# Kernel optimization log

Hardware: AMD Instinct MI355X
Metric: run time of the kernel (lower is better)

The kernel has to match this reference:

```python
import jax, jax.numpy as jnp
import numpy as np

# wav2vec2 feature-extractor conv stack config: (kernel, stride) per layer, 512 channels
CONV_CFG = [(10, 5), (3, 2), (3, 2), (3, 2), (3, 2), (2, 2), (2, 2)]
C = 512
PROJ = 256
HID = 128
NCLS = 5
N_WORDS = 64
B = 8
L = 40000


def _conv1d(h, w, stride):
    # h: [B, Cin, T], w: [Cout, Cin, K]
    return jax.lax.conv_general_dilated(
        h, w, window_strides=(stride,), padding='VALID',
        dimension_numbers=('NCH', 'OIH', 'NCH'))


def setup_inputs() -> dict:
    key = jax.random.key(0)
    ks = jax.random.split(key, 16)
    x = jax.random.normal(ks[0], (B, L), dtype=jnp.float32)
    word_ids = jax.random.randint(ks[1], (B,), 0, N_WORDS)
    convs = {}
    cin = 1
    for i, (k, s) in enumerate(CONV_CFG):
        fan = cin * k
        convs[f'conv{i}'] = jax.random.normal(ks[2 + i], (C, cin, k), dtype=jnp.float32) / np.sqrt(fan)
        cin = C
    gn_scale = jnp.ones((C,), dtype=jnp.float32)
    gn_bias = jnp.zeros((C,), dtype=jnp.float32)
    proj_w = jax.random.normal(ks[9], (PROJ, C), dtype=jnp.float32) / np.sqrt(C)
    proj_b = jnp.zeros((PROJ,), dtype=jnp.float32)
    cls_w1 = jax.random.normal(ks[10], (N_WORDS, PROJ, HID), dtype=jnp.float32) / np.sqrt(PROJ)
    cls_b1 = jnp.zeros((N_WORDS, HID), dtype=jnp.float32)
    cls_w2 = jax.random.normal(ks[11], (N_WORDS, HID, NCLS), dtype=jnp.float32) / np.sqrt(HID)
    cls_b2 = jnp.zeros((N_WORDS, NCLS), dtype=jnp.float32)
    return dict(x=x, word_ids=word_ids, gn_scale=gn_scale, gn_bias=gn_bias,
                proj_w=proj_w, proj_b=proj_b, cls_w1=cls_w1, cls_b1=cls_b1,
                cls_w2=cls_w2, cls_b2=cls_b2, **convs)


def _forward(x, convs, gn_scale, gn_bias, proj_w, proj_b, cls_w1, cls_b1, cls_w2, cls_b2, word_ids):
    h = x[:, None, :]  # [B,1,L]
    for i, (k, s) in enumerate(CONV_CFG):
        h = _conv1d(h, convs[i], s)
        if i == 0:
            # wav2vec2 group-norm: groups == channels -> per-channel norm over time
            mu = jnp.mean(h, axis=-1, keepdims=True)
            var = jnp.var(h, axis=-1, keepdims=True)
            h = (h - mu) * jax.lax.rsqrt(var + 1e-5)
            h = h * gn_scale[None, :, None] + gn_bias[None, :, None]
        h = jax.nn.gelu(h)
    feat = jnp.mean(h, axis=-1)                          # [B, 512] mean-pool over time
    feat = jax.nn.relu(feat @ proj_w.T + proj_b)         # [B, 256] (dropout = identity in eval)
    w1 = cls_w1[word_ids]                                # [B, 256, 128] routed gather
    h1 = jax.nn.relu(jnp.einsum('bd,bdh->bh', feat, w1) + cls_b1[word_ids])
    out = jnp.einsum('bh,bho->bo', h1, cls_w2[word_ids]) + cls_b2[word_ids]  # [B, 5]
    return out


def reference(x, word_ids, gn_scale, gn_bias, proj_w, proj_b, cls_w1, cls_b1, cls_w2, cls_b2,
              conv0, conv1, conv2, conv3, conv4, conv5, conv6):
    convs = [conv0, conv1, conv2, conv3, conv4, conv5, conv6]
    return _forward(x, convs, gn_scale, gn_bias, proj_w, proj_b,
                    cls_w1, cls_b1, cls_w2, cls_b2, word_ids)
```

## Files before the change

kernel.cpp:

```cpp
#include <hip/hip_runtime.h>
#include <hip/hip_bf16.h>

typedef unsigned short u16;
typedef short bf16x8 __attribute__((ext_vector_type(8)));
typedef float f32x4 __attribute__((ext_vector_type(4)));

#define CC 512

__device__ __forceinline__ float gelu_tanh(float x) {
    float x3 = x * x * x;
    float z  = 0.7978845608028654f * (x + 0.044715f * x3);
    float e  = __expf(2.0f * z);
    float th = 1.0f - 2.0f / (e + 1.0f);
    return 0.5f * x * (1.0f + th);
}

__device__ __forceinline__ u16 f2bf(float f) {
    union { float f; unsigned u; } v; v.f = f;
    unsigned r = v.u + 0x7fff + ((v.u >> 16) & 1);
    return (u16)(r >> 16);
}
__device__ __forceinline__ float bf2f(u16 h) {
    union { unsigned u; float f; } v; v.u = ((unsigned)h) << 16; return v.f;
}

__global__ __launch_bounds__(256) void conv0_store(
    const float* __restrict__ x, const float* __restrict__ w0,
    u16* __restrict__ actG, float* __restrict__ part) {
    const int t0 = blockIdx.x * 64, b = blockIdx.y;
    __shared__ float xs[64 * 5 + 16];
    __shared__ float w0t[10 * 512];
    for (int i = threadIdx.x; i < 64 * 5 + 5; i += 256) {
        int gi = t0 * 5 + i;
        xs[i] = (gi < 40000) ? x[b * 40000 + gi] : 0.0f;
    }
    for (int i = threadIdx.x; i < 5120; i += 256) {
        int c = i / 10, j = i - c * 10;
        w0t[j * 512 + c] = w0[i];
    }
    __syncthreads();
    const int lane = threadIdx.x & 63, wv = threadIdx.x >> 6;
    float wr[8][10];
#pragma unroll
    for (int q = 0; q < 8; ++q)
#pragma unroll
        for (int j = 0; j < 10; ++j) wr[q][j] = w0t[j * 512 + lane + 64 * q];
    float sacc[8] = {}, qacc[8] = {};
    u16* ob = actG + ((size_t)b * 8320 + t0 + wv * 16) * 512 + lane;
#pragma unroll
    for (int u = 0; u < 16; ++u) {
        const int tt = wv * 16 + u;
        const int t  = t0 + tt;
        float xv[10];
#pragma unroll
        for (int j = 0; j < 10; ++j) xv[j] = xs[tt * 5 + j];
#pragma unroll
        for (int q = 0; q < 8; ++q) {
            float a = 0.0f;
#pragma unroll
            for (int j = 0; j < 10; ++j) a = fmaf(wr[q][j], xv[j], a);
            const u16 h = f2bf(a);
            ob[(size_t)u * 512 + 64 * q] = h;
            if (t < 7999) {
                const float ar = bf2f(h);
                sacc[q] += ar; qacc[q] += ar * ar;
            }
        }
    }
    float* pp = part + ((((size_t)blockIdx.x * 4 + wv) * 8 + b) * 512 + lane) * 2;
#pragma unroll
    for (int q = 0; q < 8; ++q) {
        pp[q * 128] = sacc[q]; pp[q * 128 + 1] = qacc[q];
    }
}

__global__ __launch_bounds__(256) void stats_finalizeAB(
    const float* __restrict__ part, const float* __restrict__ gsc,
    const float* __restrict__ gbi, float* __restrict__ Af, float* __restrict__ Bf) {
    const int row = blockIdx.x * 256 + threadIdx.x;
    float s = 0.0f, q = 0.0f;
    for (int k = 0; k < 500; ++k) {
        const float2 v = *(const float2*)(part + ((size_t)k * 4096 + row) * 2);
        s += v.x; q += v.y;
    }
    float mean = s / 7999.0f;
    float var  = fmaxf(q / 7999.0f - mean * mean, 0.0f);
    float rstd = rsqrtf(var + 1e-5f);
    const int c = row & (CC - 1);
    float A = rstd * gsc[c];
    Af[row] = A;
    Bf[row] = gbi[c] - mean * A;
}

__global__ __launch_bounds__(256) void gn_apply(
    u16* __restrict__ actG, const float* __restrict__ Af,
    const float* __restrict__ Bf) {
    const int b = blockIdx.y;
    const int idx = blockIdx.x * 256 + threadIdx.x;
    const int row = idx >> 6, c0 = (idx & 63) * 8;
    if (row >= 7999) return;
    u16* p = actG + ((size_t)b * 8320 + row) * 512 + c0;
    union { u16 s[8]; uint4 v; } in, outv;
    in.v = *(const uint4*)p;
    const float4 a0 = *(const float4*)(Af + b * 512 + c0);
    const float4 a1 = *(const float4*)(Af + b * 512 + c0 + 4);
    const float4 b0 = *(const float4*)(Bf + b * 512 + c0);
    const float4 b1 = *(const float4*)(Bf + b * 512 + c0 + 4);
    const float av[8] = {a0.x, a0.y, a0.z, a0.w, a1.x, a1.y, a1.z, a1.w};
    const float bv[8] = {b0.x, b0.y, b0.z, b0.w, b1.x, b1.y, b1.z, b1.w};
#pragma unroll
    for (int e = 0; e < 8; ++e)
        outv.s[e] = f2bf(gelu_tanh(fmaf(bf2f(in.s[e]), av[e], bv[e])));
    *(uint4*)p = outv.v;
}

template <int K, int NL>
struct WtBatch { const float* src[NL]; u16* dst[NL]; };

template <int K, int NL>
__global__ __launch_bounds__(256) void wt_transform(WtBatch<K, NL> a) {
    constexpr int WROW = 32 * K + 8;
    const int cit = blockIdx.x, cob = blockIdx.y, l = blockIdx.z;
    const float* w = a.src[l];
    u16* dst = a.dst[l] + ((size_t)(cob * 16 + cit)) * 128 * WROW;
    for (int idx = threadIdx.x; idx < 128 * WROW; idx += 256) {
        const int co = idx / WROW, e = idx - co * WROW;
        u16 hi = 0;
        if (e < 32 * K) {
            const int j = e >> 5, ci = e & 31;
            hi = f2bf(w[((size_t)(cob * 128 + co) * 512 + cit * 32 + ci) * K + j]);
        }
        dst[idx] = hi;
    }
}

template <int K, int TT>
__global__ __launch_bounds__(256, 2) void conv_mfma(
    const u16* __restrict__ act, int capIn,
    const u16* __restrict__ wt,
    u16* __restrict__ outAct, int capOut, int tbShift) {
    constexpr int WROW = 32 * K + 8;
    constexpr int XH   = TT + 8;
    constexpr int TF   = TT / 32;
    constexpr int NXCH = XH * 8;
    constexpr int NWCH = 128 * WROW / 8;
    constexpr int NKX  = (NXCH + 255) / 256;
    constexpr int NKW  = (NWCH + 255) / 256;

    __shared__ __align__(16) u16 Xs[XH * 64];
    __shared__ __align__(16) u16 Ws[128 * WROW];

    const int tid  = threadIdx.x;
    const int lane = tid & 63;
    const int wv   = tid >> 6;
    const int wco  = wv >> 1, wtt = wv & 1;
    const int l15  = lane & 15, l16 = lane >> 4;

    const int flat = blockIdx.x;
    const int xcd  = flat & 7, cob = (flat >> 3) & 3;
    const int G    = xcd + (flat >> 5) * 8;
    const int t_b  = G & ((1 << tbShift) - 1);
    const int b    = G >> tbShift;
    const int t0   = t_b * TT;
    const int x0   = t0 * 2;

    const char* abase = (const char*)(act + (size_t)b * capIn * 512);
    const u16*  wbase = wt + (size_t)cob * (16 * 128 * WROW);

    const char* xsrc[NKX]; int xdst[NKX]; bool xok[NKX];
#pragma unroll
    for (int k = 0; k < NKX; ++k) {
        const int cb = wv * 64 + k * 256;
        xok[k] = (cb < NXCH);
        const int c  = cb + lane;
        const int xh = c >> 3;
        const int li = ((c & 7) * 16) ^ ((xh & 7) << 4);
        const int xx = min(x0 + 2 * xh + (li >> 6), capIn - 1);
        xsrc[k] = abase + (size_t)xx * 1024 + (li & 63);
        xdst[k] = cb * 16;
    }
    const char* wsrc[NKW]; int wdst[NKW]; bool wok[NKW];
#pragma unroll
    for (int k = 0; k < NKW; ++k) {
        const int cb = wv * 64 + k * 256;
        wok[k] = (cb < NWCH);
        wsrc[k] = (const char*)wbase + (size_t)(cb + lane) * 16;
        wdst[k] = cb * 16;
    }

    auto stageAll = [&]() {
#pragma unroll
        for (int k = 0; k < NKX; ++k)
            if (xok[k])
                __builtin_amdgcn_global_load_lds(
                    (const __attribute__((address_space(1))) void*)xsrc[k],
                    (__attribute__((address_space(3))) void*)((char*)&Xs[0] + xdst[k]),
                    16, 0, 0);
#pragma unroll
        for (int k = 0; k < NKW; ++k)
            if (wok[k])
                __builtin_amdgcn_global_load_lds(
                    (const __attribute__((address_space(1))) void*)wsrc[k],
                    (__attribute__((address_space(3))) void*)((char*)&Ws[0] + wdst[k]),
                    16, 0, 0);
#pragma unroll
        for (int k = 0; k < NKX; ++k) xsrc[k] += 64;
#pragma unroll
        for (int k = 0; k < NKW; ++k) wsrc[k] += 128 * WROW * 2;
    };

    int xoff[K][TF];
    int woff[K][4];
#pragma unroll
    for (int j = 0; j < K; ++j) {
#pragma unroll
        for (int tf = 0; tf < TF; ++tf) {
            const int tl = wtt * (TT / 2) + tf * 16 + l15;
            const int xl = 2 * tl + j;
            const int xh = xl >> 1, p = xl & 1;
            xoff[j][tf] = xh * 128 + ((p * 64 + l16 * 16) ^ ((xh & 7) << 4));
        }
#pragma unroll
        for (int cf = 0; cf < 4; ++cf)
            woff[j][cf] = (wco * 64 + cf * 16 + l15) * WROW + j * 32 + l16 * 8;
    }

    f32x4 acc[4][TF] = {};

    stageAll();
    __syncthreads();

#pragma unroll 1
    for (int cit = 0; cit < 16; ++cit) {
        bf16x8 xr[K][TF], wr[K][4];
#pragma unroll
        for (int j = 0; j < K; ++j) {
#pragma unroll
            for (int tf = 0; tf < TF; ++tf)
                xr[j][tf] = *(const bf16x8*)((const char*)&Xs[0] + xoff[j][tf]);
#pragma unroll
            for (int cf = 0; cf < 4; ++cf)
                wr[j][cf] = *(const bf16x8*)(&Ws[0] + woff[j][cf]);
        }
        __syncthreads();
        if (cit < 15) stageAll();
#pragma unroll
        for (int j = 0; j < K; ++j)
#pragma unroll
            for (int cf = 0; cf < 4; ++cf)
#pragma unroll
                for (int tf = 0; tf < TF; ++tf)
                    acc[cf][tf] = __builtin_amdgcn_mfma_f32_16x16x32_bf16(
                        wr[j][cf], xr[j][tf], acc[cf][tf], 0, 0, 0);
        __syncthreads();
    }

    u16* ob = outAct + (size_t)b * capOut * 512;
#pragma unroll
    for (int cf = 0; cf < 4; ++cf) {
#pragma unroll
        for (int tf = 0; tf < TF; ++tf) {
            const int tG  = t0 + wtt * (TT / 2) + tf * 16 + l15;
            const int coG = cob * 128 + wco * 64 + cf * 16 + l16 * 4;
            union { u16 s[4]; uint2 v; } pk;
#pragma unroll
            for (int r = 0; r < 4; ++r)
                pk.s[r] = f2bf(gelu_tanh(acc[cf][tf][r]));
            *(uint2*)(ob + (size_t)tG * 512 + coG) = pk.v;
        }
    }
}

__global__ __launch_bounds__(512) void feat_proj_kernel(
    const u16* __restrict__ act, int cap,
    const float* __restrict__ pw, const float* __restrict__ pb,
    float* __restrict__ pfeat) {
    const int b = blockIdx.x;
    __shared__ float fs[8][512];
    __shared__ float feat[CC];
    const int c8 = (threadIdx.x & 63) * 8;
    const int tg = threadIdx.x >> 6;
    float s[8] = {};
    for (int t = tg; t < 124; t += 8) {
        union { u16 u[8]; uint4 v; } in;
        in.v = *(const uint4*)(act + ((size_t)b * cap + t) * 512 + c8);
#pragma unroll
        for (int e = 0; e < 8; ++e) s[e] += bf2f(in.u[e]);
    }
#pragma unroll
    for (int e = 0; e < 8; ++e) fs[tg][c8 + e] = s[e];
    __syncthreads();
    {
        const int c = threadIdx.x;
        if (c < 512) {
            float acc = 0.0f;
#pragma unroll
            for (int g = 0; g < 8; ++g) acc += fs[g][c];
            feat[c] = acc * (1.0f / 124.0f);
        }
    }
    __syncthreads();
    if (threadIdx.x < 256) {
        const int j = threadIdx.x;
        const float* wr = pw + (size_t)j * CC;
        float acc = pb[j];
        for (int cc = 0; cc < CC; ++cc) acc = fmaf(feat[cc], wr[cc], acc);
        pfeat[b * 256 + j] = fmaxf(acc, 0.0f);
    }
}

__global__ __launch_bounds__(128) void cls_kernel(
    const float* __restrict__ pfeat, const int* __restrict__ wid,
    const float* __restrict__ w1, const float* __restrict__ b1,
    const float* __restrict__ w2, const float* __restrict__ b2,
    float* __restrict__ out) {
    const int b = blockIdx.x;
    const int id = wid[b];
    __shared__ float pf[256], h1[128];
    for (int d = threadIdx.x; d < 256; d += 128) pf[d] = pfeat[b * 256 + d];
    __syncthreads();
    {
        const int hh = threadIdx.x;
        const float* w1p = w1 + (size_t)id * 256 * 128;
        float s = b1[id * 128 + hh];
        for (int d = 0; d < 256; ++d) s = fmaf(pf[d], w1p[d * 128 + hh], s);
        h1[hh] = fmaxf(s, 0.0f);
    }
    __syncthreads();
    if (threadIdx.x < 5) {
        const float* w2p = w2 + (size_t)id * 128 * 5;
        float s = b2[id * 5 + threadIdx.x];
        for (int hh = 0; hh < 128; ++hh) s = fmaf(h1[hh], w2p[hh * 5 + threadIdx.x], s);
        out[b * 5 + threadIdx.x] = s;
    }
}

extern "C" void kernel_launch(void* const* d_in, const int* in_sizes, int n_in,
                              void* d_out, int out_size, void* d_ws, size_t ws_size,
                              hipStream_t stream) {
    const float* x   = (const float*)d_in[0];
    const int*   wid = (const int*)d_in[1];
    const float* gsc = (const float*)d_in[2];
    const float* gbi = (const float*)d_in[3];
    const float* pw  = (const float*)d_in[4];
    const float* pb  = (const float*)d_in[5];
    const float* w1  = (const float*)d_in[6];
    const float* b1  = (const float*)d_in[7];
    const float* w2  = (const float*)d_in[8];
    const float* b2  = (const float*)d_in[9];
    const float* cw[7];
    for (int i = 0; i < 7; ++i) cw[i] = (const float*)d_in[10 + i];

    char* ws = (char*)d_ws;
    const size_t SZ_ACTG = (size_t)8 * 8320 * 512 * 2;
    const size_t SZ_P    = (size_t)8 * 4224 * 512 * 2;
    const size_t SZ_Q    = (size_t)8 * 2176 * 512 * 2;
    u16* actG = (u16*)ws;
    u16* bufP = (u16*)(ws + SZ_ACTG);
    u16* bufQ = (u16*)(ws + SZ_ACTG + SZ_P);
    size_t off = SZ_ACTG + SZ_P + SZ_Q;
    u16* wtbuf[7];
    for (int i = 1; i <= 4; ++i) { wtbuf[i] = (u16*)(ws + off); off += (size_t)4 * 16 * 128 * 104 * 2; }
    for (int i = 5; i <= 6; ++i) { wtbuf[i] = (u16*)(ws + off); off += (size_t)4 * 16 * 128 * 72 * 2; }
    off = (off + 255) & ~(size_t)255;
    float* statsPart = (float*)(ws + off); off += (size_t)500 * 8 * 512 * 2 * 4;
    float* Af        = (float*)(ws + off); off += 4096 * 4;
    float* Bf        = (float*)(ws + off); off += 4096 * 4;
    float* pfeat     = (float*)(ws + off); off += 8 * 256 * 4;

    conv0_store<<<dim3(125, 8), 256, 0, stream>>>(x, cw[0], actG, statsPart);
    stats_finalizeAB<<<dim3(16), 256, 0, stream>>>(statsPart, gsc, gbi, Af, Bf);
    gn_apply<<<dim3(2000, 8), 256, 0, stream>>>(actG, Af, Bf);

    {
        WtBatch<3, 4> a;
        for (int i = 0; i < 4; ++i) { a.src[i] = cw[1 + i]; a.dst[i] = wtbuf[1 + i]; }
        wt_transform<3, 4><<<dim3(16, 4, 4), 256, 0, stream>>>(a);
        WtBatch<2, 2> c;
        for (int i = 0; i < 2; ++i) { c.src[i] = cw[5 + i]; c.dst[i] = wtbuf[5 + i]; }
        wt_transform<2, 2><<<dim3(16, 4, 2), 256, 0, stream>>>(c);
    }

    conv_mfma<3, 128><<<dim3(32 * 32), 256, 0, stream>>>(actG, 8320, wtbuf[1], bufP, 4224, 5);
    conv_mfma<3, 128><<<dim3(16 * 32), 256, 0, stream>>>(bufP, 4224, wtbuf[2], bufQ, 2176, 4);
    conv_mfma<3,  64><<<dim3(16 * 32), 256, 0, stream>>>(bufQ, 2176, wtbuf[3], bufP, 4224, 4);
    conv_mfma<3,  64><<<dim3( 8 * 32), 256, 0, stream>>>(bufP, 4224, wtbuf[4], bufQ, 2176, 3);
    conv_mfma<2,  64><<<dim3( 4 * 32), 256, 0, stream>>>(bufQ, 2176, wtbuf[5], bufP, 4224, 2);
    conv_mfma<2,  64><<<dim3( 2 * 32), 256, 0, stream>>>(bufP, 4224, wtbuf[6], bufQ, 2176, 1);

    feat_proj_kernel<<<dim3(8), 512, 0, stream>>>(bufQ, 2176, pw, pb, pfeat);
    cls_kernel<<<dim3(8), 128, 0, stream>>>(pfeat, wid, w1, b1, w2, b2, (float*)d_out);
}
```

Measured before the change: 317.8 us.

## Double-buffer activation tiles and use fine-grained vmcnt waits in conv MFMA loop

Splits the activation LDS tile into two buffers so the next-next input-channel chunk of X is prefetched while the current chunk is consumed. Replaces the per-iteration __syncthreads with explicit lgkmcnt/vmcnt waits plus raw barriers, letting outstanding X loads stay in flight across iterations. It also repartitions the async global-to-LDS copy work evenly across waves. This doubles X LDS use, which may affect occupancy at 2 blocks per CU, and the hand-computed vmcnt immediate must match the issue order.

```diff
diff --git a/kernel.cpp b/kernel.cpp
--- a/kernel.cpp
+++ b/kernel.cpp
@@ -6,6 +6,10 @@
 typedef float f32x4 __attribute__((ext_vector_type(4)));
 
 #define CC 512
+
+constexpr int vmimm(int n) {
+    return (n & 0xF) | ((n >> 4) << 14) | (0x7 << 4) | (0xF << 8);
+}
 
 __device__ __forceinline__ float gelu_tanh(float x) {
     float x3 = x * x * x;
@@ -142,12 +146,16 @@
     constexpr int WROW = 32 * K + 8;
     constexpr int XH   = TT + 8;
     constexpr int TF   = TT / 32;
-    constexpr int NXCH = XH * 8;
-    constexpr int NWCH = 128 * WROW / 8;
-    constexpr int NKX  = (NXCH + 255) / 256;
-    constexpr int NKW  = (NWCH + 255) / 256;
-
-    __shared__ __align__(16) u16 Xs[XH * 64];
+    constexpr int TXC  = XH * 8;
+    constexpr int CPX  = TXC / 4;
+    constexpr int NIX  = (CPX + 63) / 64;
+    constexpr int XLAST = CPX - (NIX - 1) * 64;
+    constexpr int TWC  = 128 * WROW / 8;
+    constexpr int CPW  = TWC / 4;
+    constexpr int NIW  = (CPW + 63) / 64;
+    constexpr int WLAST = CPW - (NIW - 1) * 64;
+
+    __shared__ __align__(16) u16 Xs[2][XH * 64];
     __shared__ __align__(16) u16 Ws[128 * WROW];
 
     const int tid  = threadIdx.x;
@@ -167,46 +175,45 @@
     const char* abase = (const char*)(act + (size_t)b * capIn * 512);
     const u16*  wbase = wt + (size_t)cob * (16 * 128 * WROW);
 
-    const char* xsrc[NKX]; int xdst[NKX]; bool xok[NKX];
-#pragma unroll
-    for (int k = 0; k < NKX; ++k) {
-        const int cb = wv * 64 + k * 256;
-        xok[k] = (cb < NXCH);
-        const int c  = cb + lane;
+    const char* xsA[NIX]; const char* xsB[NIX]; int xdst[NIX];
+#pragma unroll
+    for (int i = 0; i < NIX; ++i) {
+        const int c  = wv * CPX + i * 64 + lane;
         const int xh = c >> 3;
         const int li = ((c & 7) * 16) ^ ((xh & 7) << 4);
         const int xx = min(x0 + 2 * xh + (li >> 6), capIn - 1);
-        xsrc[k] = abase + (size_t)xx * 1024 + (li & 63);
-        xdst[k] = cb * 16;
-    }
-    const char* wsrc[NKW]; int wdst[NKW]; bool wok[NKW];
-#pragma unroll
-    for (int k = 0; k < NKW; ++k) {
-        const int cb = wv * 64 + k * 256;
-        wok[k] = (cb < NWCH);
-        wsrc[k] = (const char*)wbase + (size_t)(cb + lane) * 16;
-        wdst[k] = cb * 16;
-    }
-
-    auto stageAll = [&]() {
-#pragma unroll
-        for (int k = 0; k < NKX; ++k)
-            if (xok[k])
+        xsA[i] = abase + (size_t)xx * 1024 + (li & 63);
+        xsB[i] = xsA[i] + 64;
+        xdst[i] = (wv * CPX + i * 64) * 16;
+    }
+    const char* wsrc[NIW]; int wdst[NIW];
+#pragma unroll
+    for (int i = 0; i < NIW; ++i) {
+        wsrc[i] = (const char*)wbase + (size_t)(wv * CPW + i * 64 + lane) * 16;
+        wdst[i] = (wv * CPW + i * 64) * 16;
+    }
+
+    auto stageX = [&](const char* (&xs)[NIX], u16* xb) {
+#pragma unroll
+        for (int i = 0; i < NIX; ++i)
+            if (i < NIX - 1 || lane < XLAST)
                 __builtin_amdgcn_global_load_lds(
-                    (const __attribute__((address_space(1))) void*)xsrc[k],
-                    (__attribute__((address_space(3))) void*)((char*)&Xs[0] + xdst[k]),
+                    (const __attribute__((address_space(1))) void*)xs[i],
+                    (__attribute__((address_space(3))) void*)((char*)xb + xdst[i]),
                     16, 0, 0);
 #pragma unroll
-        for (int k = 0; k < NKW; ++k)
-            if (wok[k])
+        for (int i = 0; i < NIX; ++i) xs[i] += 128;
+    };
+    auto stageW = [&]() {
+#pragma unroll
+        for (int i = 0; i < NIW; ++i)
+            if (i < NIW - 1 || lane < WLAST)
                 __builtin_amdgcn_global_load_lds(
-                    (const __attribute__((address_space(1))) void*)wsrc[k],
-                    (__attribute__((address_space(3))) void*)((char*)&Ws[0] + wdst[k]),
+                    (const __attribute__((address_space(1))) void*)wsrc[i],
+                    (__attribute__((address_space(3))) void*)((char*)&Ws[0] + wdst[i]),
                     16, 0, 0);
 #pragma unroll
-        for (int k = 0; k < NKX; ++k) xsrc[k] += 64;
-#pragma unroll
-        for (int k = 0; k < NKW; ++k) wsrc[k] += 128 * WROW * 2;
+        for (int i = 0; i < NIW; ++i) wsrc[i] += WROW * 256;
     };
 
     int xoff[K][TF];
@@ -222,28 +229,31 @@
         }
 #pragma unroll
         for (int cf = 0; cf < 4; ++cf)
-            woff[j][cf] = (wco * 64 + cf * 16 + l15) * WROW + j * 32 + l16 * 8;
+            woff[j][cf] = ((wco * 64 + cf * 16 + l15) * WROW + j * 32 + l16 * 8) * 2;
     }
 
     f32x4 acc[4][TF] = {};
 
-    stageAll();
-    __syncthreads();
-
-#pragma unroll 1
-    for (int cit = 0; cit < 16; ++cit) {
+    stageX(xsA, &Xs[0][0]);
+    stageX(xsB, &Xs[1][0]);
+    stageW();
+    __syncthreads();
+
+    auto body = [&](int cit, u16* xb, const char* (&xset)[NIX]) {
         bf16x8 xr[K][TF], wr[K][4];
 #pragma unroll
         for (int j = 0; j < K; ++j) {
 #pragma unroll
             for (int tf = 0; tf < TF; ++tf)
-                xr[j][tf] = *(const bf16x8*)((const char*)&Xs[0] + xoff[j][tf]);
+                xr[j][tf] = *(const bf16x8*)((const char*)xb + xoff[j][tf]);
 #pragma unroll
             for (int cf = 0; cf < 4; ++cf)
-                wr[j][cf] = *(const bf16x8*)(&Ws[0] + woff[j][cf]);
-        }
-        __syncthreads();
-        if (cit < 15) stageAll();
+                wr[j][cf] = *(const bf16x8*)((const char*)&Ws[0] + woff[j][cf]);
+        }
+        asm volatile("s_waitcnt lgkmcnt(0)" ::: "memory");
+        __builtin_amdgcn_s_barrier();
+        if (cit < 15) stageW();
+        if (cit < 14) stageX(xset, xb);
 #pragma unroll
         for (int j = 0; j < K; ++j)
 #pragma unroll
@@ -252,7 +262,19 @@
                 for (int tf = 0; tf < TF; ++tf)
                     acc[cf][tf] = __builtin_amdgcn_mfma_f32_16x16x32_bf16(
                         wr[j][cf], xr[j][tf], acc[cf][tf], 0, 0, 0);
-        __syncthreads();
+        if (cit < 14) {
+            __builtin_amdgcn_s_waitcnt(vmimm(NIX));
+            __builtin_amdgcn_s_barrier();
+        } else if (cit == 14) {
+            __builtin_amdgcn_s_waitcnt(vmimm(0));
+            __builtin_amdgcn_s_barrier();
+        }
+    };
+
+#pragma unroll 1
+    for (int c2 = 0; c2 < 16; c2 += 2) {
+        body(c2,     &Xs[0][0], xsA);
+        body(c2 + 1, &Xs[1][0], xsB);
     }
 
     u16* ob = outAct + (size_t)b * capOut * 512;
```

New measurement: 315.6 us. Within noise of the previous version (-0.7%).
